# Kernel optimization log

Hardware: AMD Instinct MI355X
Metric: run time of the kernel (lower is better)

Reference implementation:

```python
import jax, jax.numpy as jnp
import numpy as np

EPS = 1e-6
INPUTS = 1836
LABELS = 159
NUM_VALS = 2
HIDDEN = 1024
BATCH = 8192
ITERS = 20          # cfg.inference.iterations
INF_LR = 1.0        # cfg.inference.learning_rate (sqrt decay)
ENT_COEF = 1.0      # cfg.entropy_coef


def setup_inputs() -> dict:
    key = jax.random.key(0)
    ks = jax.random.split(key, 8)
    f32 = jnp.float32
    xs = jax.random.normal(ks[0], (BATCH, INPUTS), f32)
    # feature MLP: 1836 -> 150 -> 150 -> 159 (weights ~ N(0, 2/fan_in), bias 0)
    Wf1 = jax.random.normal(ks[1], (150, INPUTS), f32) * np.sqrt(2.0 / INPUTS).astype(np.float32)
    bf1 = jnp.zeros((150,), f32)
    Wf2 = jax.random.normal(ks[2], (150, 150), f32) * np.sqrt(2.0 / 150).astype(np.float32)
    bf2 = jnp.zeros((150,), f32)
    Wf3 = jax.random.normal(ks[3], (LABELS, 150), f32) * np.sqrt(2.0 / 150).astype(np.float32)
    bf3 = jnp.zeros((LABELS,), f32)
    # global energy net: Linear(159->1024, no bias), Softplus, Linear(1024->1, no bias)
    Wg1 = jax.random.normal(ks[4], (HIDDEN, LABELS), f32) * (1.0 / np.sqrt(LABELS)).astype(np.float32)
    Wg2 = jax.random.normal(ks[5], (1, HIDDEN), f32) * (1.0 / np.sqrt(HIDDEN)).astype(np.float32)
    return dict(xs=xs, Wf1=Wf1, bf1=bf1, Wf2=Wf2, bf2=bf2, Wf3=Wf3, bf3=bf3, Wg1=Wg1, Wg2=Wg2)


def _init_pred(batch_size):
    # _random_probabilities: sorted-uniform stick-breaking, shared across the batch
    x = jax.random.uniform(jax.random.key(1), (LABELS, NUM_VALS + 1), jnp.float32)
    x = x.at[:, 0].set(0.0).at[:, -1].set(1.0)
    x = jnp.sort(x, axis=1)
    p = x[:, 1:] - x[:, :-1]                       # (LABELS, NUM_VALS), rows sum to 1
    return jnp.broadcast_to(p[None], (batch_size, LABELS, NUM_VALS))


def reference(xs, Wf1, bf1, Wf2, bf2, Wf3, bf3, Wg1, Wg2):
    # feature energy network -> potentials (B, LABELS, 2), channel 0 is zero
    h = jax.nn.relu(xs @ Wf1.T + bf1)
    h = jax.nn.relu(h @ Wf2.T + bf2)
    logits = h @ Wf3.T + bf3                        # (B, LABELS)
    potentials = jnp.stack([jnp.zeros_like(logits), logits], axis=-1)  # (B, LABELS, 2)

    def energy_sum(pred):
        # sum over batch of: <pred, potentials> + Wg2 softplus(Wg1 pred[:,:,1]) - c*H-term
        ge = jnp.sum(pred * potentials)
        le = jnp.sum(jax.nn.softplus(pred[:, :, 1] @ Wg1.T) @ Wg2.T)
        ent = jnp.sum(pred * jnp.log(pred + EPS))
        return ge + le - ENT_COEF * ent

    egrad = jax.grad(energy_sum)

    def step(pred, it):
        g = egrad(pred)                             # (B, LABELS, NUM_VALS)
        lr = INF_LR / jnp.sqrt(it.astype(jnp.float32))
        lg = lr * g
        m = jnp.max(lg, axis=-1, keepdims=True)     # stabilized multiplicative update
        p = pred * jnp.exp(lg - m)
        p = p / (jnp.sum(p, axis=-1, keepdims=True) + EPS)
        return p, None

    pred0 = _init_pred(xs.shape[0])
    pred, _ = jax.lax.scan(step, pred0, jnp.arange(1, ITERS))
    return pred
```

## Files before the change

### kernel.cpp

```cpp
#include <hip/hip_runtime.h>
#include <hip/hip_bf16.h>
#include <math.h>

#define EPSF 1e-6f
#define NLBL 159
#define NLP  160
#define HID  1024
#define BATCH 8192
#define MROWS 32
#define PBS  168
#define SBS  1044
#define K1   1836
#define K1P  1856
#define NF   150
#define NFP  160

typedef __attribute__((ext_vector_type(8))) short short8v;
typedef __attribute__((ext_vector_type(4))) float f32x4;

__device__ inline ushort f2bf(float f) {
  __hip_bfloat16 h = __float2bfloat16(f);
  return *reinterpret_cast<ushort*>(&h);
}
__device__ inline float bf2f(ushort u) {
  unsigned v = ((unsigned)u) << 16;
  return __uint_as_float(v);
}
__device__ inline float rcpf(float x) { return __builtin_amdgcn_rcpf(x); }
__device__ inline float sigmoidf(float x) { return rcpf(1.0f + __expf(-x)); }

__device__ inline unsigned rotl32(unsigned x, int d){ return (x<<d)|(x>>(32-d)); }

__device__ inline void threefry2x32(unsigned k0, unsigned k1,
                                    unsigned x0, unsigned x1,
                                    unsigned* o0, unsigned* o1) {
  unsigned ks0=k0, ks1=k1, ks2=k0^k1^0x1BD11BDAu;
  x0 += ks0; x1 += ks1;
#define TF_R(r) { x0 += x1; x1 = rotl32(x1,(r)); x1 ^= x0; }
  TF_R(13) TF_R(15) TF_R(26) TF_R(6)  x0 += ks1; x1 += ks2 + 1u;
  TF_R(17) TF_R(29) TF_R(16) TF_R(24) x0 += ks2; x1 += ks0 + 2u;
  TF_R(13) TF_R(15) TF_R(26) TF_R(6)  x0 += ks0; x1 += ks1 + 3u;
  TF_R(17) TF_R(29) TF_R(16) TF_R(24) x0 += ks1; x1 += ks2 + 4u;
  TF_R(13) TF_R(15) TF_R(26) TF_R(6)  x0 += ks2; x1 += ks0 + 5u;
#undef TF_R
  *o0 = x0; *o1 = x1;
}

template<int RELU>
__global__ __launch_bounds__(256) void gemm_xwt(const float* __restrict__ A,
                                                const float* __restrict__ W,
                                                const float* __restrict__ bias,
                                                float* __restrict__ C,
                                                int M, int N, int K) {
  __shared__ float As[32][68];
  __shared__ float Ws[32][68];
  const int tid = threadIdx.x;
  const int m0 = blockIdx.x * 64;
  const int n0 = blockIdx.y * 64;
  const int tn = tid & 15;
  const int tm = tid >> 4;
  float acc[4][4];
#pragma unroll
  for (int i=0;i<4;++i)
#pragma unroll
    for (int j=0;j<4;++j) acc[i][j]=0.f;

  for (int k0 = 0; k0 < K; k0 += 32) {
    __syncthreads();
#pragma unroll
    for (int s2 = 0; s2 < 8; ++s2) {
      int f = tid + s2*256;
      int kk = f & 31, mm = f >> 5;
      int k = k0 + kk;
      float av = 0.f, wvv = 0.f;
      if (k < K) {
        av = A[(size_t)(m0+mm)*K + k];
        int n = n0 + mm;
        if (n < N) wvv = W[(size_t)n*K + k];
      }
      As[kk][mm] = av;
      Ws[kk][mm] = wvv;
    }
    __syncthreads();
    for (int kk=0; kk<32; ++kk) {
      float4 a4 = *(const float4*)&As[kk][tm*4];
      float4 b4 = *(const float4*)&Ws[kk][tn*4];
      float ai[4] = {a4.x,a4.y,a4.z,a4.w};
      float bj[4] = {b4.x,b4.y,b4.z,b4.w};
#pragma unroll
      for (int i=0;i<4;++i)
#pragma unroll
        for (int j=0;j<4;++j) acc[i][j] = fmaf(ai[i], bj[j], acc[i][j]);
    }
  }
#pragma unroll
  for (int i=0;i<4;++i)
#pragma unroll
    for (int j=0;j<4;++j) {
      int m = m0 + tm*4 + i;
      int n = n0 + tn*4 + j;
      if (n < N) {
        float v = acc[i][j] + bias[n];
        if (RELU) v = fmaxf(v, 0.f);
        C[(size_t)m*N + n] = v;
      }
    }
}

__global__ void prep_weights(const float* __restrict__ Wg1,
                             ushort* __restrict__ Wg1b,
                             ushort* __restrict__ Wg1Tb) {
  int idx = blockIdx.x*256 + threadIdx.x;
  if (idx >= HID*NLP) return;
  int h = idx / NLP, l = idx % NLP;
  float v = (l < NLBL) ? Wg1[h*NLBL + l] : 0.f;
  ushort b = f2bf(v);
  Wg1b[h*NLP + l]  = b;
  Wg1Tb[l*HID + h] = b;
}

__global__ void prep_wf1(const float* __restrict__ Wf1,
                         ushort* __restrict__ Wh, ushort* __restrict__ Wl) {
  int idx = blockIdx.x*256 + threadIdx.x;
  if (idx >= NFP*K1P) return;
  int n = idx / K1P, k = idx % K1P;
  float v = (n < NF && k < K1) ? Wf1[n*K1 + k] : 0.f;
  ushort h = f2bf(v);
  Wh[idx] = h;
  Wl[idx] = f2bf(v - bf2f(h));
}

__global__ __launch_bounds__(256) void gemm1_split(
    const float* __restrict__ xs, const ushort* __restrict__ Wh,
    const ushort* __restrict__ Wl, const float* __restrict__ bias,
    float* __restrict__ h1) {
  __shared__ float Asf[32*36];
  const int tid = threadIdx.x;
  const int wv = tid >> 6, lane = tid & 63;
  const int c = lane & 15, g = lane >> 4;
  const int row0 = blockIdx.x * 32;
  const int ntc = (wv < 2) ? 3 : 2;
  const int ntv[3] = {wv, wv + 4, wv + 8};

  f32x4 acc[3][2];
#pragma unroll
  for (int t = 0; t < 3; ++t)
#pragma unroll
    for (int rt = 0; rt < 2; ++rt) acc[t][rt] = (f32x4){0.f,0.f,0.f,0.f};

  const int srow = tid >> 3;
  const int skof = (tid & 7) * 4;

  for (int ks = 0; ks < K1P/32; ++ks) {
    const int k0 = ks * 32;
    const int ksrc = k0 + skof;
    const float4 av = *(const float4*)&xs[(size_t)(row0 + srow)*K1 + ((ksrc < K1) ? ksrc : 0)];
    __syncthreads();
    *(float4*)&Asf[srow*36 + skof] = av;
    __syncthreads();
    short8v ah[2], al[2];
#pragma unroll
    for (int rt = 0; rt < 2; ++rt) {
      const float* ap = &Asf[(rt*16 + c)*36 + g*8];
      float4 x0 = *(const float4*)ap;
      float4 x1 = *(const float4*)(ap + 4);
      float xv[8] = {x0.x,x0.y,x0.z,x0.w,x1.x,x1.y,x1.z,x1.w};
#pragma unroll
      for (int j = 0; j < 8; ++j) {
        ushort hh = f2bf(xv[j]);
        ah[rt][j] = (short)hh;
        al[rt][j] = (short)f2bf(xv[j] - bf2f(hh));
      }
    }
#pragma unroll
    for (int t = 0; t < 3; ++t) {
      if (t >= ntc) break;
      const int n = ntv[t]*16 + c;
      const size_t wo = (size_t)n*K1P + k0 + g*8;
      short8v wh = *(const short8v*)&Wh[wo];
      short8v wl = *(const short8v*)&Wl[wo];
#pragma unroll
      for (int rt = 0; rt < 2; ++rt) {
        acc[t][rt] = __builtin_amdgcn_mfma_f32_16x16x32_bf16(ah[rt], wh, acc[t][rt], 0, 0, 0);
        acc[t][rt] = __builtin_amdgcn_mfma_f32_16x16x32_bf16(ah[rt], wl, acc[t][rt], 0, 0, 0);
        acc[t][rt] = __builtin_amdgcn_mfma_f32_16x16x32_bf16(al[rt], wh, acc[t][rt], 0, 0, 0);
      }
    }
  }
#pragma unroll
  for (int t = 0; t < 3; ++t) {
    if (t >= ntc) break;
    const int n = ntv[t]*16 + c;
    if (n < NF) {
      const float bv = bias[n];
#pragma unroll
      for (int rt = 0; rt < 2; ++rt)
#pragma unroll
        for (int r = 0; r < 4; ++r) {
          int m = row0 + rt*16 + g*4 + r;
          h1[(size_t)m*NF + n] = fmaxf(acc[t][rt][r] + bv, 0.f);
        }
    }
  }
}

__global__ __launch_bounds__(512, 2) void spen_iter_mfma(
    const float* __restrict__ logits,
    const ushort* __restrict__ Wg1b,
    const ushort* __restrict__ Wg1Tb,
    const float* __restrict__ Wg2,
    float* __restrict__ out) {
  __shared__ ushort p1b[MROWS*PBS];
  __shared__ ushort s_b[MROWS*SBS];
  __shared__ float  u_s[NLBL];

  const int tid  = threadIdx.x;
  const int wv   = tid >> 6;
  const int lane = tid & 63;
  const int col  = lane & 15;
  const int kg   = lane >> 4;
  const int row0 = blockIdx.x * MROWS;
  const int rot  = (int)((blockIdx.x >> 3) & 7u);

  if (tid < NLBL) {
    unsigned i = 3u*(unsigned)tid + 1u;
    unsigned x0, x1; bool use1;
    if (i < 239u) { x0 = i; x1 = (i == 238u) ? 0u : (239u + i); use1 = false; }
    else          { x0 = i - 239u; x1 = i; use1 = true; }
    unsigned o0, o1;
    threefry2x32(0u, 1u, x0, x1, &o0, &o1);
    unsigned bits = use1 ? o1 : o0;
    u_s[tid] = __uint_as_float((bits >> 9) | 0x3f800000u) - 1.0f;
  }
  __syncthreads();
  for (int idx = tid; idx < MROWS*NLP; idx += 512) {
    int m = idx / NLP, l = idx % NLP;
    float p1 = (l < NLBL) ? (1.0f - u_s[l]) : 0.f;
    p1b[m*PBS + l] = f2bf(p1);
  }

  const int rgA = (wv + rot) & 7;
  const int tB  = (wv + rot) & 7;
  const bool has2 = (tB < 2);
  const int l0 = tB*16 + col;
  const int l1 = 128 + tB*16 + col;
  const bool v1 = has2 && (l1 < NLBL);

  float q0[8], q1[8];
  {
    float u0v = u_s[l0];
    float qi0 = __logf((1.0f - u0v) * rcpf(u0v));
    float qi1 = 0.f;
    if (v1) { float u1v = u_s[l1]; qi1 = __logf((1.0f - u1v) * rcpf(u1v)); }
#pragma unroll
    for (int i = 0; i < 8; ++i) { q0[i] = qi0; q1[i] = qi1; }
  }

  float wg2own[8];
#pragma unroll
  for (int j = 0; j < 8; ++j) wg2own[j] = Wg2[(rgA*8 + j)*16 + col];

  float lg0[8], lg1[8];
#pragma unroll
  for (int rh = 0; rh < 2; ++rh)
#pragma unroll
    for (int r = 0; r < 4; ++r) {
      int m = row0 + rh*16 + kg*4 + r;
      lg0[rh*4+r] = logits[(size_t)m*NLBL + l0];
      lg1[rh*4+r] = v1 ? logits[(size_t)m*NLBL + l1] : 0.f;
    }

  const ushort* wbase = Wg1b + ((size_t)(rgA*128) + col)*NLP + kg*8;
  const ushort* sp0 = &s_b[col*SBS + kg*8];
  const ushort* sp1 = &s_b[(16 + col)*SBS + kg*8];
  const ushort* wt0 = &Wg1Tb[(size_t)l0*HID + kg*8];
  const ushort* wt1 = &Wg1Tb[(size_t)l1*HID + kg*8];

  for (int it = 1; it <= 19; ++it) {
    const float lr = rsqrtf((float)it);
    __syncthreads();
    short8v afr0[5], afr1[5];
#pragma unroll
    for (int kk = 0; kk < 5; ++kk) {
      afr0[kk] = *(const short8v*)&p1b[col*PBS + kk*32 + kg*8];
      afr1[kk] = *(const short8v*)&p1b[(16 + col)*PBS + kk*32 + kg*8];
    }
    short8v wA[2][5];
#pragma unroll
    for (int kk = 0; kk < 5; ++kk) wA[0][kk] = *(const short8v*)(wbase + kk*32);
#pragma unroll
    for (int j = 0; j < 8; ++j) {
      const int cur = j & 1;
      if (j < 7) {
        const ushort* p = wbase + (size_t)((j + 1)*16)*NLP;
#pragma unroll
        for (int kk = 0; kk < 5; ++kk) wA[cur^1][kk] = *(const short8v*)(p + kk*32);
      }
      f32x4 a0 = (f32x4){0.f,0.f,0.f,0.f};
      f32x4 a1 = (f32x4){0.f,0.f,0.f,0.f};
#pragma unroll
      for (int kk = 0; kk < 5; ++kk) {
        a0 = __builtin_amdgcn_mfma_f32_16x16x32_bf16(afr0[kk], wA[cur][kk], a0, 0, 0, 0);
        a1 = __builtin_amdgcn_mfma_f32_16x16x32_bf16(afr1[kk], wA[cur][kk], a1, 0, 0, 0);
      }
      const int h = (rgA*8 + j)*16 + col;
      const float g = wg2own[j];
#pragma unroll
      for (int r = 0; r < 4; ++r) {
        s_b[(kg*4 + r)*SBS + h]      = f2bf(g * sigmoidf(a0[r]));
        s_b[(16 + kg*4 + r)*SBS + h] = f2bf(g * sigmoidf(a1[r]));
      }
    }
    __syncthreads();
    f32x4 bA0 = (f32x4){0.f,0.f,0.f,0.f};
    f32x4 bA1 = (f32x4){0.f,0.f,0.f,0.f};
    f32x4 bB0 = (f32x4){0.f,0.f,0.f,0.f};
    f32x4 bB1 = (f32x4){0.f,0.f,0.f,0.f};
    if (has2) {
      short8v wr[2][2][4];
#pragma unroll
      for (int j = 0; j < 4; ++j) {
        wr[0][0][j] = *(const short8v*)(wt0 + j*32);
        wr[0][1][j] = *(const short8v*)(wt1 + j*32);
      }
#pragma unroll
      for (int b = 0; b < 8; ++b) {
        const int cur = b & 1;
        if (b < 7) {
#pragma unroll
          for (int j = 0; j < 4; ++j) {
            wr[cur^1][0][j] = *(const short8v*)(wt0 + ((b+1)*4 + j)*32);
            wr[cur^1][1][j] = *(const short8v*)(wt1 + ((b+1)*4 + j)*32);
          }
        }
#pragma unroll
        for (int j = 0; j < 4; ++j) {
          const int kk = b*4 + j;
          short8v a0 = *(const short8v*)(sp0 + kk*32);
          short8v a1 = *(const short8v*)(sp1 + kk*32);
          bA0 = __builtin_amdgcn_mfma_f32_16x16x32_bf16(a0, wr[cur][0][j], bA0, 0, 0, 0);
          bA1 = __builtin_amdgcn_mfma_f32_16x16x32_bf16(a1, wr[cur][0][j], bA1, 0, 0, 0);
          bB0 = __builtin_amdgcn_mfma_f32_16x16x32_bf16(a0, wr[cur][1][j], bB0, 0, 0, 0);
          bB1 = __builtin_amdgcn_mfma_f32_16x16x32_bf16(a1, wr[cur][1][j], bB1, 0, 0, 0);
        }
      }
    } else {
      short8v wr[2][4];
#pragma unroll
      for (int j = 0; j < 4; ++j)
        wr[0][j] = *(const short8v*)(wt0 + j*32);
#pragma unroll
      for (int b = 0; b < 8; ++b) {
        const int cur = b & 1;
        if (b < 7) {
#pragma unroll
          for (int j = 0; j < 4; ++j)
            wr[cur^1][j] = *(const short8v*)(wt0 + ((b+1)*4 + j)*32);
        }
#pragma unroll
        for (int j = 0; j < 4; ++j) {
          const int kk = b*4 + j;
          short8v a0 = *(const short8v*)(sp0 + kk*32);
          short8v a1 = *(const short8v*)(sp1 + kk*32);
          bA0 = __builtin_amdgcn_mfma_f32_16x16x32_bf16(a0, wr[cur][j], bA0, 0, 0, 0);
          bA1 = __builtin_amdgcn_mfma_f32_16x16x32_bf16(a1, wr[cur][j], bA1, 0, 0, 0);
        }
      }
    }
#define UPDATE_ONE(QARR, IDX, LGV, BK, LL, MM)                               \
    {                                                                        \
      float q = QARR[IDX];                                                   \
      float p1v = sigmoidf(q);                                               \
      float p0v = 1.0f - p1v;                                                \
      float rp1 = rcpf(p1v + EPSF);                                          \
      float rp0 = rcpf(p0v + EPSF);                                          \
      float dlt = (LGV) + (BK) - __logf((p1v + EPSF)*rp0) - p1v*rp1 + p0v*rp0;\
      q += lr*dlt;                                                           \
      QARR[IDX] = q;                                                         \
      p1b[(MM)*PBS + (LL)] = f2bf(sigmoidf(q));                              \
    }
#pragma unroll
    for (int r = 0; r < 4; ++r) {
      const int m0r = kg*4 + r;
      UPDATE_ONE(q0, r, lg0[r], bA0[r], l0, m0r)
      const int m1r = 16 + kg*4 + r;
      UPDATE_ONE(q0, 4 + r, lg0[4 + r], bA1[r], l0, m1r)
    }
    if (v1) {
#pragma unroll
      for (int r = 0; r < 4; ++r) {
        const int m0r = kg*4 + r;
        UPDATE_ONE(q1, r, lg1[r], bB0[r], l1, m0r)
        const int m1r = 16 + kg*4 + r;
        UPDATE_ONE(q1, 4 + r, lg1[4 + r], bB1[r], l1, m1r)
      }
    }
#undef UPDATE_ONE
  }

#pragma unroll
  for (int rh = 0; rh < 2; ++rh)
#pragma unroll
    for (int r = 0; r < 4; ++r) {
      const int row = row0 + rh*16 + kg*4 + r;
      float p1v = sigmoidf(q0[rh*4 + r]);
      size_t o = ((size_t)row*NLBL + l0)*2;
      out[o]   = 1.0f - p1v;
      out[o+1] = p1v;
      if (v1) {
        float p1w = sigmoidf(q1[rh*4 + r]);
        size_t o2 = ((size_t)row*NLBL + l1)*2;
        out[o2]   = 1.0f - p1w;
        out[o2+1] = p1w;
      }
    }
}

extern "C" void kernel_launch(void* const* d_in, const int* in_sizes, int n_in,
                              void* d_out, int out_size, void* d_ws, size_t ws_size,
                              hipStream_t stream) {
  const float* xs  = (const float*)d_in[0];
  const float* Wf1 = (const float*)d_in[1];
  const float* bf1 = (const float*)d_in[2];
  const float* Wf2 = (const float*)d_in[3];
  const float* bf2 = (const float*)d_in[4];
  const float* Wf3 = (const float*)d_in[5];
  const float* bf3 = (const float*)d_in[6];
  const float* Wg1 = (const float*)d_in[7];
  const float* Wg2 = (const float*)d_in[8];
  float* out = (float*)d_out;

  float* h1     = (float*)d_ws;
  float* h2     = h1 + (size_t)BATCH*NF;
  float* logits = h2 + (size_t)BATCH*NF;
  ushort* Wg1b  = (ushort*)(logits + (size_t)BATCH*NLBL);
  ushort* Wg1Tb = Wg1b + (size_t)HID*NLP;
  ushort* Wf1h  = Wg1Tb + (size_t)NLP*HID;
  ushort* Wf1l  = Wf1h + (size_t)NFP*K1P;

  prep_wf1<<<(NFP*K1P + 255)/256, 256, 0, stream>>>(Wf1, Wf1h, Wf1l);
  prep_weights<<<(HID*NLP + 255)/256, 256, 0, stream>>>(Wg1, Wg1b, Wg1Tb);

  gemm1_split<<<BATCH/32, 256, 0, stream>>>(xs, Wf1h, Wf1l, bf1, h1);
  gemm_xwt<1><<<dim3(BATCH/64, 3), 256, 0, stream>>>(h1, Wf2, bf2, h2, BATCH, NF, NF);
  gemm_xwt<0><<<dim3(BATCH/64, 3), 256, 0, stream>>>(h2, Wf3, bf3, logits, BATCH, NLBL, NF);

  spen_iter_mfma<<<BATCH/MROWS, 512, 0, stream>>>(logits, Wg1b, Wg1Tb, Wg2, out);
}
```

Before: 526.3 us.

## Stream Wg1 tiles into an LDS double-buffered ring via global_load_lds

Replaces per-wave register prefetch of Wg1 in the first GEMM with asynchronous global-to-LDS DMA loads into a two-slot ring, gated by explicit vmcnt waits. Each wave now handles interleaved hidden columns (c*128 + wv*16) instead of a block-rotated contiguous range, and the first tile of the next iteration is prefetched during the second GEMM. Tile loads for Wg1T are hoisted before the barrier. This aims to cut register pressure and hide global load latency, but adds about 80KB of LDS per block, which likely limits occupancy below the 2 blocks per CU requested by the launch bounds, and drops the per-block rotation that spread access across cache lines.

```diff
diff --git a/kernel.cpp b/kernel.cpp
--- a/kernel.cpp
+++ b/kernel.cpp
@@ -28,6 +28,12 @@
 }
 __device__ inline float rcpf(float x) { return __builtin_amdgcn_rcpf(x); }
 __device__ inline float sigmoidf(float x) { return rcpf(1.0f + __expf(-x)); }
+
+__device__ __forceinline__ void dma16(const void* g, void* l) {
+  __builtin_amdgcn_global_load_lds(
+      (const __attribute__((address_space(1))) unsigned int*)g,
+      (__attribute__((address_space(3))) unsigned int*)l, 16, 0, 0);
+}
 
 __device__ inline unsigned rotl32(unsigned x, int d){ return (x<<d)|(x>>(32-d)); }
 
@@ -210,6 +216,7 @@
     const ushort* __restrict__ Wg1Tb,
     const float* __restrict__ Wg2,
     float* __restrict__ out) {
+  __shared__ __align__(16) ushort ring[2][20480];
   __shared__ ushort p1b[MROWS*PBS];
   __shared__ ushort s_b[MROWS*SBS];
   __shared__ float  u_s[NLBL];
@@ -220,7 +227,6 @@
   const int col  = lane & 15;
   const int kg   = lane >> 4;
   const int row0 = blockIdx.x * MROWS;
-  const int rot  = (int)((blockIdx.x >> 3) & 7u);
 
   if (tid < NLBL) {
     unsigned i = 3u*(unsigned)tid + 1u;
@@ -239,11 +245,9 @@
     p1b[m*PBS + l] = f2bf(p1);
   }
 
-  const int rgA = (wv + rot) & 7;
-  const int tB  = (wv + rot) & 7;
-  const bool has2 = (tB < 2);
-  const int l0 = tB*16 + col;
-  const int l1 = 128 + tB*16 + col;
+  const bool has2 = (wv < 2);
+  const int l0 = wv*16 + col;
+  const int l1 = 128 + wv*16 + col;
   const bool v1 = has2 && (l1 < NLBL);
 
   float q0[8], q1[8];
@@ -258,7 +262,7 @@
 
   float wg2own[8];
 #pragma unroll
-  for (int j = 0; j < 8; ++j) wg2own[j] = Wg2[(rgA*8 + j)*16 + col];
+  for (int c = 0; c < 8; ++c) wg2own[c] = Wg2[(c*8 + wv)*16 + col];
 
   float lg0[8], lg1[8];
 #pragma unroll
@@ -270,12 +274,19 @@
       lg1[rh*4+r] = v1 ? logits[(size_t)m*NLBL + l1] : 0.f;
     }
 
-  const ushort* wbase = Wg1b + ((size_t)(rgA*128) + col)*NLP + kg*8;
+  const char* wg1b_bytes = (const char*)Wg1b;
   const ushort* sp0 = &s_b[col*SBS + kg*8];
   const ushort* sp1 = &s_b[(16 + col)*SBS + kg*8];
   const ushort* wt0 = &Wg1Tb[(size_t)l0*HID + kg*8];
   const ushort* wt1 = &Wg1Tb[(size_t)l1*HID + kg*8];
 
+  {
+    const char* g = wg1b_bytes + wv*5120 + lane*16;
+#pragma unroll
+    for (int i = 0; i < 5; ++i)
+      dma16(g + i*1024, (char*)&ring[0][wv*2560] + i*1024);
+  }
+
   for (int it = 1; it <= 19; ++it) {
     const float lr = rsqrtf((float)it);
     __syncthreads();
@@ -285,52 +296,63 @@
       afr0[kk] = *(const short8v*)&p1b[col*PBS + kk*32 + kg*8];
       afr1[kk] = *(const short8v*)&p1b[(16 + col)*PBS + kk*32 + kg*8];
     }
-    short8v wA[2][5];
-#pragma unroll
-    for (int kk = 0; kk < 5; ++kk) wA[0][kk] = *(const short8v*)(wbase + kk*32);
-#pragma unroll
-    for (int j = 0; j < 8; ++j) {
-      const int cur = j & 1;
-      if (j < 7) {
-        const ushort* p = wbase + (size_t)((j + 1)*16)*NLP;
-#pragma unroll
-        for (int kk = 0; kk < 5; ++kk) wA[cur^1][kk] = *(const short8v*)(p + kk*32);
-      }
+#pragma unroll
+    for (int c = 0; c < 8; ++c) {
+      if (c < 7) {
+        const char* g = wg1b_bytes + (size_t)(c+1)*40960 + wv*5120 + lane*16;
+        char* l = (char*)&ring[(c+1)&1][wv*2560];
+#pragma unroll
+        for (int i = 0; i < 5; ++i)
+          dma16(g + i*1024, l + i*1024);
+        asm volatile("s_waitcnt vmcnt(5)" ::: "memory");
+      } else {
+        asm volatile("s_waitcnt vmcnt(0)" ::: "memory");
+      }
+      __builtin_amdgcn_sched_barrier(0);
+      const ushort* wtile = &ring[c&1][wv*2560];
       f32x4 a0 = (f32x4){0.f,0.f,0.f,0.f};
       f32x4 a1 = (f32x4){0.f,0.f,0.f,0.f};
 #pragma unroll
       for (int kk = 0; kk < 5; ++kk) {
-        a0 = __builtin_amdgcn_mfma_f32_16x16x32_bf16(afr0[kk], wA[cur][kk], a0, 0, 0, 0);
-        a1 = __builtin_amdgcn_mfma_f32_16x16x32_bf16(afr1[kk], wA[cur][kk], a1, 0, 0, 0);
-      }
-      const int h = (rgA*8 + j)*16 + col;
-      const float g = wg2own[j];
+        short8v bf = *(const short8v*)&wtile[col*160 + kk*32 + kg*8];
+        a0 = __builtin_amdgcn_mfma_f32_16x16x32_bf16(afr0[kk], bf, a0, 0, 0, 0);
+        a1 = __builtin_amdgcn_mfma_f32_16x16x32_bf16(afr1[kk], bf, a1, 0, 0, 0);
+      }
+      const int h = c*128 + wv*16 + col;
+      const float g2 = wg2own[c];
 #pragma unroll
       for (int r = 0; r < 4; ++r) {
-        s_b[(kg*4 + r)*SBS + h]      = f2bf(g * sigmoidf(a0[r]));
-        s_b[(16 + kg*4 + r)*SBS + h] = f2bf(g * sigmoidf(a1[r]));
-      }
-    }
-    __syncthreads();
+        s_b[(kg*4 + r)*SBS + h]      = f2bf(g2 * sigmoidf(a0[r]));
+        s_b[(16 + kg*4 + r)*SBS + h] = f2bf(g2 * sigmoidf(a1[r]));
+      }
+    }
+    short8v wrA[2][4], wrB[2][4];
+#pragma unroll
+    for (int j = 0; j < 4; ++j) wrA[0][j] = *(const short8v*)(wt0 + j*32);
+    if (has2) {
+#pragma unroll
+      for (int j = 0; j < 4; ++j) wrB[0][j] = *(const short8v*)(wt1 + j*32);
+    }
+    __syncthreads();
+    if (it < 19) {
+      const char* g = wg1b_bytes + wv*5120 + lane*16;
+#pragma unroll
+      for (int i = 0; i < 5; ++i)
+        dma16(g + i*1024, (char*)&ring[0][wv*2560] + i*1024);
+    }
     f32x4 bA0 = (f32x4){0.f,0.f,0.f,0.f};
     f32x4 bA1 = (f32x4){0.f,0.f,0.f,0.f};
     f32x4 bB0 = (f32x4){0.f,0.f,0.f,0.f};
     f32x4 bB1 = (f32x4){0.f,0.f,0.f,0.f};
     if (has2) {
-      short8v wr[2][2][4];
-#pragma unroll
-      for (int j = 0; j < 4; ++j) {
-        wr[0][0][j] = *(const short8v*)(wt0 + j*32);
-        wr[0][1][j] = *(const short8v*)(wt1 + j*32);
-      }
 #pragma unroll
       for (int b = 0; b < 8; ++b) {
         const int cur = b & 1;
         if (b < 7) {
 #pragma unroll
           for (int j = 0; j < 4; ++j) {
-            wr[cur^1][0][j] = *(const short8v*)(wt0 + ((b+1)*4 + j)*32);
-            wr[cur^1][1][j] = *(const short8v*)(wt1 + ((b+1)*4 + j)*32);
+            wrA[cur^1][j] = *(const short8v*)(wt0 + ((b+1)*4 + j)*32);
+            wrB[cur^1][j] = *(const short8v*)(wt1 + ((b+1)*4 + j)*32);
           }
         }
 #pragma unroll
@@ -338,32 +360,28 @@
           const int kk = b*4 + j;
           short8v a0 = *(const short8v*)(sp0 + kk*32);
           short8v a1 = *(const short8v*)(sp1 + kk*32);
-          bA0 = __builtin_amdgcn_mfma_f32_16x16x32_bf16(a0, wr[cur][0][j], bA0, 0, 0, 0);
-          bA1 = __builtin_amdgcn_mfma_f32_16x16x32_bf16(a1, wr[cur][0][j], bA1, 0, 0, 0);
-          bB0 = __builtin_amdgcn_mfma_f32_16x16x32_bf16(a0, wr[cur][1][j], bB0, 0, 0, 0);
-          bB1 = __builtin_amdgcn_mfma_f32_16x16x32_bf16(a1, wr[cur][1][j], bB1, 0, 0, 0);
+          bA0 = __builtin_amdgcn_mfma_f32_16x16x32_bf16(a0, wrA[cur][j], bA0, 0, 0, 0);
+          bA1 = __builtin_amdgcn_mfma_f32_16x16x32_bf16(a1, wrA[cur][j], bA1, 0, 0, 0);
+          bB0 = __builtin_amdgcn_mfma_f32_16x16x32_bf16(a0, wrB[cur][j], bB0, 0, 0, 0);
+          bB1 = __builtin_amdgcn_mfma_f32_16x16x32_bf16(a1, wrB[cur][j], bB1, 0, 0, 0);
         }
       }
     } else {
-      short8v wr[2][4];
-#pragma unroll
-      for (int j = 0; j < 4; ++j)
-        wr[0][j] = *(const short8v*)(wt0 + j*32);
 #pragma unroll
       for (int b = 0; b < 8; ++b) {
         const int cur = b & 1;
         if (b < 7) {
 #pragma unroll
           for (int j = 0; j < 4; ++j)
-            wr[cur^1][j] = *(const short8v*)(wt0 + ((b+1)*4 + j)*32);
+            wrA[cur^1][j] = *(const short8v*)(wt0 + ((b+1)*4 + j)*32);
         }
 #pragma unroll
         for (int j = 0; j < 4; ++j) {
           const int kk = b*4 + j;
           short8v a0 = *(const short8v*)(sp0 + kk*32);
           short8v a1 = *(const short8v*)(sp1 + kk*32);
-          bA0 = __builtin_amdgcn_mfma_f32_16x16x32_bf16(a0, wr[cur][j], bA0, 0, 0, 0);
-          bA1 = __builtin_amdgcn_mfma_f32_16x16x32_bf16(a1, wr[cur][j], bA1, 0, 0, 0);
+          bA0 = __builtin_amdgcn_mfma_f32_16x16x32_bf16(a0, wrA[cur][j], bA0, 0, 0, 0);
+          bA1 = __builtin_amdgcn_mfma_f32_16x16x32_bf16(a1, wrA[cur][j], bA1, 0, 0, 0);
         }
       }
     }
```

Measured after the change: 511.7 us. 1.03x faster.
